# Optimization experiments

Measured on AMD Instinct MI355X. Metric: run time of the kernel, lower is better.

Reference implementation:

```python
import jax, jax.numpy as jnp
import numpy as np

B, T, C, DD = 32, 2048, 32, 8  # batch, time steps, value channels, demo channels


def setup_inputs() -> dict:
    key = jax.random.key(0)
    k1, k2, k3, k4 = jax.random.split(key, 4)
    demo = jax.random.normal(k1, (B, DD), dtype=jnp.float32)
    times = jax.random.uniform(k2, (B, T), dtype=jnp.float32)
    values = jax.random.normal(k3, (B, T, C), dtype=jnp.float32)
    measurements = jax.random.randint(k4, (B, T, C), 0, 2) > 0
    return {"demo": demo, "times": times, "values": values, "measurements": measurements}


def reference(demo, times, values, measurements):
    # Faithful dense-packed version of the TF per-channel ragged pack:
    # for each channel c, observed (time, one_hot(c), value) triples are packed
    # to the front of each batch row (tf.where + stable sort on batch id keeps
    # within-row time order); rows with zero observations get one all-zero pad
    # entry (csd = -1 -> one_hot gives zeros), which dense zero-padding subsumes.
    b, t, c = values.shape
    dd = demo.shape[-1]
    depth = dd + c          # one-hot depth, as in build()
    F = depth + 2           # [time, one_hot(depth), value]
    dt = values.dtype

    mask = measurements
    maskf = mask.astype(dt)
    # packed position of each observed (b, t, c) within its (b, c) row
    pos = jnp.cumsum(mask.astype(jnp.int32), axis=1) - 1          # [B,T,C]
    pos_safe = jnp.where(mask, pos, t)                            # dump slot t

    onehot_c = jnp.eye(depth, dtype=dt)[:c]                       # [C, depth]
    feat = jnp.concatenate([
        (times[:, :, None] * maskf)[..., None],                   # time  [B,T,C,1]
        maskf[..., None] * onehot_c[None, None],                  # csd   [B,T,C,depth]
        (values * maskf)[..., None],                              # value [B,T,C,1]
    ], axis=-1)                                                   # [B,T,C,F]

    cI = jnp.broadcast_to(jnp.arange(c)[None, None, :], (b, t, c))
    bI = jnp.broadcast_to(jnp.arange(b)[:, None, None], (b, t, c))
    out = jnp.zeros((c, b, t + 1, F), dtype=dt)
    out = out.at[cI, bI, pos_safe].add(feat)                      # unique except dump
    packed = out[:, :, :t]                                        # [C,B,T,F]

    # demo channels: one entry per row, time=0, one_hot index = C + x - 1 (as in source)
    idx = c + jnp.arange(dd) - 1                                  # [DD]
    oh = jnp.eye(depth, dtype=dt)[idx]                            # [DD, depth]
    demo_row = jnp.concatenate([
        jnp.zeros((dd, b, 1), dtype=dt),                          # time = 0
        jnp.broadcast_to(oh[:, None, :], (dd, b, depth)),         # one-hot
        demo.T[..., None],                                        # value
    ], axis=-1)                                                   # [DD,B,F]
    demo_full = jnp.zeros((dd, b, t, F), dtype=dt).at[:, :, 0, :].set(demo_row)

    return jnp.concatenate([packed, demo_full], axis=0)           # [C+DD,B,T,F]
```

## Files before the change

kernel.cpp:

```cpp
#include <hip/hip_runtime.h>
#include <stdint.h>

#define BB 32
#define TT 2048
#define CC 32
#define DDIM 8
#define FF 42
#define SLAB_B (TT * FF)
#define SLAB_CH (BB * SLAB_B)
#define TOTAL (40L * SLAB_CH)

__device__ __forceinline__ int read_mask(const void* meas, size_t idx, int mode) {
    if (mode == 3) return ((const unsigned long long*)meas)[idx] != 0ull;
    if (mode == 1) return ((const uint8_t*)meas)[idx] != 0;
    if (mode == 2) return ((const unsigned short*)meas)[idx] != 0;
    return ((const unsigned*)meas)[idx] != 0u;
}

__device__ __forceinline__ int block_detect_mask_mode(const void* meas,
                                                      unsigned* s_A, unsigned* s_Aodd) {
    if (threadIdx.x == 0) { *s_A = 0u; *s_Aodd = 0u; }
    __syncthreads();
    if (threadIdx.x < 256) {
        unsigned w = ((const unsigned*)meas)[threadIdx.x];
        atomicOr(s_A, w);
        if (threadIdx.x & 1) atomicOr(s_Aodd, w);
    }
    __syncthreads();
    unsigned A = *s_A, Aodd = *s_Aodd;
    unsigned hi = A >> 24;
    if (hi == 0u) return (Aodd == 0u) ? 3 : 0;
    if (hi >= 0x3Cu && hi <= 0x3Fu) return (A & 0xFFFFu) ? 2 : 0;
    return 1;
}

__global__ __launch_bounds__(512)
void compact_kernel(const float* __restrict__ demo,
                    const float* __restrict__ times,
                    const float* __restrict__ values,
                    const void* __restrict__ meas,
                    float* __restrict__ ws_time,
                    float* __restrict__ ws_val,
                    int* __restrict__ count,
                    float* __restrict__ ws_demo) {
    __shared__ unsigned s_A, s_Aodd;
    __shared__ int s_wcnt[8];
    const int mode = block_detect_mask_mode(meas, &s_A, &s_Aodd);

    const int bid = blockIdx.x;
    const int c = bid >> 5, b = bid & 31;
    const int w = threadIdx.x >> 6;
    const int lane = threadIdx.x & 63;
    const int tbase = w * 256;

    if (bid == 0 && threadIdx.x < BB * DDIM)
        ws_demo[threadIdx.x] = demo[threadIdx.x];

    int mycnt = 0;
#pragma unroll
    for (int i = 0; i < 4; ++i) {
        int t = tbase + i * 64 + lane;
        size_t idx = (size_t)(b * TT + t) * CC + c;
        mycnt += __popcll(__ballot(read_mask(meas, idx, mode)));
    }
    if (lane == 0) s_wcnt[w] = mycnt;
    __syncthreads();

    int base = 0;
#pragma unroll
    for (int i = 0; i < 8; ++i) if (i < w) base += s_wcnt[i];
    if (threadIdx.x == 0) {
        int tot = 0;
#pragma unroll
        for (int i = 0; i < 8; ++i) tot += s_wcnt[i];
        count[bid] = tot;
    }

    float* wt = ws_time + (size_t)bid * TT;
    float* wv = ws_val + (size_t)bid * TT;

    int kbase = base;
#pragma unroll
    for (int i = 0; i < 4; ++i) {
        int t = tbase + i * 64 + lane;
        size_t idx = (size_t)(b * TT + t) * CC + c;
        int m = read_mask(meas, idx, mode);
        unsigned long long bits = __ballot(m);
        if (m) {
            int pos = kbase + __popcll(bits & ((1ull << lane) - 1ull));
            wt[pos] = times[(size_t)b * TT + t];
            wv[pos] = values[idx];
        }
        kbase += __popcll(bits);
    }
}

template <bool HASWS>
__global__ __launch_bounds__(256)
void fill_kernel(const float* __restrict__ ws_demo,
                 const float* __restrict__ demo_raw,
                 const float* __restrict__ ws_time,
                 const float* __restrict__ ws_val,
                 const int* __restrict__ count,
                 float* __restrict__ out) {
    unsigned g = blockIdx.x * 256u + threadIdx.x;
    if (g >= (unsigned)(TOTAL / 8)) return;
    unsigned j = g * 8u;
    unsigned ch = j / (unsigned)SLAB_CH;
    unsigned r = j - ch * (unsigned)SLAB_CH;
    unsigned b = r / (unsigned)SLAB_B;
    unsigned q = r - b * (unsigned)SLAB_B;
    int k = (int)(q / (unsigned)FF);
    int f = (int)(q - (unsigned)k * FF);

    float o[8];
    if (ch < CC) {
        int cnt = HASWS ? count[ch * BB + b] : 0;
        const float* wt = ws_time + (size_t)(ch * BB + b) * TT;
        const float* wv = ws_val + (size_t)(ch * BB + b) * TT;
        int onef = 1 + (int)ch;
#pragma unroll
        for (int s = 0; s < 8; ++s) {
            float v = 0.0f;
            if (k < cnt) {
                if (f == 0) v = wt[k];
                else if (f == onef) v = 1.0f;
                else if (f == 41) v = wv[k];
            }
            o[s] = v;
            if (++f == FF) { f = 0; ++k; }
        }
    } else {
        int d = (int)ch - CC;
        float dv = HASWS ? ws_demo[b * DDIM + d] : demo_raw[(size_t)b * DDIM + d];
#pragma unroll
        for (int s = 0; s < 8; ++s) {
            float v = 0.0f;
            if (k == 0) {
                if (f == 32 + d) v = 1.0f;
                else if (f == 41) v = dv;
            }
            o[s] = v;
            if (++f == FF) { f = 0; ++k; }
        }
    }
    float4* dst = reinterpret_cast<float4*>(out) + (size_t)g * 2;
    dst[0] = make_float4(o[0], o[1], o[2], o[3]);
    dst[1] = make_float4(o[4], o[5], o[6], o[7]);
}

__global__ void scatter_kernel(const float* __restrict__ times,
                               const float* __restrict__ values,
                               const void* __restrict__ meas,
                               float* __restrict__ out) {
    __shared__ unsigned s_A, s_Aodd;
    const int mode = block_detect_mask_mode(meas, &s_A, &s_Aodd);

    int wid = (int)((blockIdx.x * blockDim.x + threadIdx.x) >> 6);
    int lane = (int)(threadIdx.x & 63);
    if (wid >= BB * CC) return;
    int b = wid / CC, c = wid % CC;

    float* base = out + (size_t)(c * BB + b) * SLAB_B;

    int kbase = 0;
    for (int t0 = 0; t0 < TT; t0 += 64) {
        int t = t0 + lane;
        size_t idx = (size_t)(b * TT + t) * CC + c;
        int m = read_mask(meas, idx, mode);
        unsigned long long bits = __ballot(m);
        if (m) {
            int pos = kbase + __popcll(bits & ((1ull << lane) - 1ull));
            float* row = base + (size_t)pos * FF;
            row[0] = times[(size_t)b * TT + t];
            row[1 + c] = 1.0f;
            row[41] = values[idx];
        }
        kbase += __popcll(bits);
    }
}

extern "C" void kernel_launch(void* const* d_in, const int* in_sizes, int n_in,
                              void* d_out, int out_size, void* d_ws, size_t ws_size,
                              hipStream_t stream) {
    const float* demo   = (const float*)d_in[0];
    const float* times  = (const float*)d_in[1];
    const float* values = (const float*)d_in[2];
    const void*  meas   = d_in[3];
    float* out = (float*)d_out;

    const size_t n_cb = (size_t)CC * BB;
    const size_t ws_need = 2 * n_cb * TT * sizeof(float)
                         + n_cb * sizeof(int)
                         + (size_t)BB * DDIM * sizeof(float);
    const int fill_blocks = (int)(TOTAL / 8 / 256);
    const int scan_blocks = (BB * CC * 64 + 255) / 256;

    if (ws_size >= ws_need) {
        float* ws_time = (float*)d_ws;
        float* ws_val  = ws_time + n_cb * TT;
        int* count     = (int*)(ws_val + n_cb * TT);
        float* ws_demo = (float*)(count + n_cb);
        compact_kernel<<<BB * CC, 512, 0, stream>>>(demo, times, values, meas,
                                                    ws_time, ws_val, count, ws_demo);
        fill_kernel<true><<<fill_blocks, 256, 0, stream>>>(ws_demo, nullptr,
                                                           ws_time, ws_val, count, out);
    } else {
        fill_kernel<false><<<fill_blocks, 256, 0, stream>>>(nullptr, demo,
                                                            nullptr, nullptr, nullptr, out);
        scatter_kernel<<<scan_blocks, 256, 0, stream>>>(times, values, meas, out);
    }
}
```

Baseline: 470.4 us.

## Split compaction into count, scan, compact passes with coalesced mask reads

Replaces the per-(channel,batch) compaction kernel, whose mask and value reads were strided by the channel count, with three kernels. A count kernel reads contiguous time chunks across all channels, a single-block scan computes chunk offsets, and a compact kernel re-reads the chunk and uses a bit-transposition to get per-channel prefixes. The goal is coalesced mask and value loads. The cost is two extra launches, a second mask read, and some register-heavy bit manipulation; the fill kernel, which dominates output writes, is unchanged.

```diff
diff --git a/kernel.cpp b/kernel.cpp
--- a/kernel.cpp
+++ b/kernel.cpp
@@ -9,6 +9,7 @@
 #define SLAB_B (TT * FF)
 #define SLAB_CH (BB * SLAB_B)
 #define TOTAL (40L * SLAB_CH)
+#define NTC 8
 
 __device__ __forceinline__ int read_mask(const void* meas, size_t idx, int mode) {
     if (mode == 3) return ((const unsigned long long*)meas)[idx] != 0ull;
@@ -35,63 +36,89 @@
 }
 
 __global__ __launch_bounds__(512)
-void compact_kernel(const float* __restrict__ demo,
-                    const float* __restrict__ times,
+void count_kernel(const void* __restrict__ meas, int* __restrict__ chunkcnt) {
+    __shared__ unsigned s_A, s_Aodd;
+    __shared__ int s_cnt[512];
+    const int mode = block_detect_mask_mode(meas, &s_A, &s_Aodd);
+
+    const int b = blockIdx.x >> 3, tc = blockIdx.x & (NTC - 1);
+    const size_t chunkbase = ((size_t)b * TT + tc * 256) * CC;
+
+    unsigned M = 0;
+#pragma unroll
+    for (int i = 0; i < 16; ++i)
+        M |= (unsigned)read_mask(meas, chunkbase + i * 512 + threadIdx.x, mode) << i;
+    s_cnt[threadIdx.x] = __popc(M);
+    __syncthreads();
+
+    if (threadIdx.x < CC) {
+        int c = threadIdx.x, sum = 0;
+#pragma unroll
+        for (int s = 0; s < 16; ++s) sum += s_cnt[s * 32 + c];
+        chunkcnt[(c * BB + b) * NTC + tc] = sum;
+    }
+}
+
+__global__ __launch_bounds__(1024)
+void scan_kernel(const int* __restrict__ chunkcnt, int* __restrict__ chunkoff,
+                 int* __restrict__ count,
+                 const float* __restrict__ demo, float* __restrict__ ws_demo) {
+    int cb = threadIdx.x;
+    int base = 0;
+#pragma unroll
+    for (int tc = 0; tc < NTC; ++tc) {
+        chunkoff[cb * NTC + tc] = base;
+        base += chunkcnt[cb * NTC + tc];
+    }
+    count[cb] = base;
+    if (threadIdx.x < BB * DDIM) ws_demo[threadIdx.x] = demo[threadIdx.x];
+}
+
+__global__ __launch_bounds__(512)
+void compact_kernel(const float* __restrict__ times,
                     const float* __restrict__ values,
                     const void* __restrict__ meas,
+                    const int* __restrict__ chunkoff,
                     float* __restrict__ ws_time,
-                    float* __restrict__ ws_val,
-                    int* __restrict__ count,
-                    float* __restrict__ ws_demo) {
+                    float* __restrict__ ws_val) {
     __shared__ unsigned s_A, s_Aodd;
-    __shared__ int s_wcnt[8];
+    __shared__ unsigned s_M[512];
     const int mode = block_detect_mask_mode(meas, &s_A, &s_Aodd);
 
-    const int bid = blockIdx.x;
-    const int c = bid >> 5, b = bid & 31;
-    const int w = threadIdx.x >> 6;
-    const int lane = threadIdx.x & 63;
-    const int tbase = w * 256;
-
-    if (bid == 0 && threadIdx.x < BB * DDIM)
-        ws_demo[threadIdx.x] = demo[threadIdx.x];
-
-    int mycnt = 0;
-#pragma unroll
-    for (int i = 0; i < 4; ++i) {
-        int t = tbase + i * 64 + lane;
-        size_t idx = (size_t)(b * TT + t) * CC + c;
-        mycnt += __popcll(__ballot(read_mask(meas, idx, mode)));
-    }
-    if (lane == 0) s_wcnt[w] = mycnt;
-    __syncthreads();
-
-    int base = 0;
-#pragma unroll
-    for (int i = 0; i < 8; ++i) if (i < w) base += s_wcnt[i];
-    if (threadIdx.x == 0) {
-        int tot = 0;
-#pragma unroll
-        for (int i = 0; i < 8; ++i) tot += s_wcnt[i];
-        count[bid] = tot;
-    }
-
-    float* wt = ws_time + (size_t)bid * TT;
-    float* wv = ws_val + (size_t)bid * TT;
-
-    int kbase = base;
-#pragma unroll
-    for (int i = 0; i < 4; ++i) {
-        int t = tbase + i * 64 + lane;
-        size_t idx = (size_t)(b * TT + t) * CC + c;
-        int m = read_mask(meas, idx, mode);
-        unsigned long long bits = __ballot(m);
-        if (m) {
-            int pos = kbase + __popcll(bits & ((1ull << lane) - 1ull));
+    const int b = blockIdx.x >> 3, tc = blockIdx.x & (NTC - 1);
+    const size_t chunkbase = ((size_t)b * TT + tc * 256) * CC;
+    const int s = threadIdx.x >> 5, c = threadIdx.x & 31;
+
+    unsigned M = 0;
+#pragma unroll
+    for (int i = 0; i < 16; ++i)
+        M |= (unsigned)read_mask(meas, chunkbase + i * 512 + threadIdx.x, mode) << i;
+    s_M[threadIdx.x] = M;
+    __syncthreads();
+
+    unsigned W[16];
+#pragma unroll
+    for (int i = 0; i < 16; ++i) W[i] = 0;
+#pragma unroll
+    for (int s2 = 0; s2 < 16; ++s2) {
+        unsigned m2 = s_M[s2 * 32 + c];
+#pragma unroll
+        for (int i = 0; i < 16; ++i) W[i] |= ((m2 >> i) & 1u) << s2;
+    }
+
+    float* wt = ws_time + (size_t)(c * BB + b) * TT;
+    float* wv = ws_val + (size_t)(c * BB + b) * TT;
+    int prefix = chunkoff[(c * BB + b) * NTC + tc];
+    const unsigned lanemask = (1u << s) - 1u;
+#pragma unroll
+    for (int i = 0; i < 16; ++i) {
+        if ((M >> i) & 1u) {
+            int pos = prefix + __popc(W[i] & lanemask);
+            int t = tc * 256 + i * 16 + s;
             wt[pos] = times[(size_t)b * TT + t];
-            wv[pos] = values[idx];
-        }
-        kbase += __popcll(bits);
+            wv[pos] = values[(size_t)(b * TT + t) * CC + c];
+        }
+        prefix += __popc(W[i]);
     }
 }
 
@@ -192,6 +219,7 @@
     const size_t n_cb = (size_t)CC * BB;
     const size_t ws_need = 2 * n_cb * TT * sizeof(float)
                          + n_cb * sizeof(int)
+                         + 2 * n_cb * NTC * sizeof(int)
                          + (size_t)BB * DDIM * sizeof(float);
     const int fill_blocks = (int)(TOTAL / 8 / 256);
     const int scan_blocks = (BB * CC * 64 + 255) / 256;
@@ -200,9 +228,14 @@
         float* ws_time = (float*)d_ws;
         float* ws_val  = ws_time + n_cb * TT;
         int* count     = (int*)(ws_val + n_cb * TT);
-        float* ws_demo = (float*)(count + n_cb);
-        compact_kernel<<<BB * CC, 512, 0, stream>>>(demo, times, values, meas,
-                                                    ws_time, ws_val, count, ws_demo);
+        int* chunkcnt  = count + n_cb;
+        int* chunkoff  = chunkcnt + n_cb * NTC;
+        float* ws_demo = (float*)(chunkoff + n_cb * NTC);
+
+        count_kernel<<<BB * NTC, 512, 0, stream>>>(meas, chunkcnt);
+        scan_kernel<<<1, 1024, 0, stream>>>(chunkcnt, chunkoff, count, demo, ws_demo);
+        compact_kernel<<<BB * NTC, 512, 0, stream>>>(times, values, meas, chunkoff,
+                                                     ws_time, ws_val);
         fill_kernel<true><<<fill_blocks, 256, 0, stream>>>(ws_demo, nullptr,
                                                            ws_time, ws_val, count, out);
     } else {
```

New measurement: 475.4 us. Within noise of the previous version (+1.0%).
